# Kernel optimization log

Hardware: AMD Instinct MI355X
Metric: run time of the kernel (lower is better)

## Reference

```python
import jax, jax.numpy as jnp
import numpy as np

N, E = 50000, 640000          # nodes, edges
F_IN, HID, CLS = 128, 128, 64  # feature dims


def setup_inputs() -> dict:
    key = jax.random.key(0)
    ks = jax.random.split(key, 12)
    x = jax.random.normal(ks[0], (N, F_IN), dtype=jnp.float32)
    edge_index = jax.random.randint(ks[1], (2, E), 0, N, dtype=jnp.int32)
    s_in = 1.0 / np.sqrt(F_IN)
    s_h = 1.0 / np.sqrt(HID)
    return {
        "x": x,
        "edge_index": edge_index,
        "W0": jax.random.normal(ks[2], (F_IN, HID), jnp.float32) * s_in,
        "b0": jnp.zeros((HID,), jnp.float32),
        "W1": jax.random.normal(ks[3], (HID, HID), jnp.float32) * s_h,
        "b1": jnp.zeros((HID,), jnp.float32),
        "W2": jax.random.normal(ks[4], (HID, HID), jnp.float32) * s_h,
        "b2": jnp.zeros((HID,), jnp.float32),
        "W_lin": jax.random.normal(ks[5], (HID, CLS), jnp.float32) * s_h,
        "b_lin": jnp.zeros((CLS,), jnp.float32),
    }


def reference(x, edge_index, W0, b0, W1, b1, W2, b2, W_lin, b_lin):
    # GCNConv (PyG defaults): out = D^-1/2 (A + I) D^-1/2 (x @ W) + b
    row, col = edge_index[0], edge_index[1]  # source -> target
    # degree with self-loop (graph is fixed across layers, compute norms once)
    deg = jnp.zeros((N,), x.dtype).at[col].add(1.0) + 1.0
    dinv = jax.lax.rsqrt(deg)                 # deg >= 1, safe
    enorm = (dinv[row] * dinv[col])[:, None]  # [E,1] edge norm
    snorm = (dinv * dinv)[:, None]            # [N,1] self-loop norm

    def conv(h, W, b):
        h = h @ W                                             # [N,HID]
        agg = jnp.zeros_like(h).at[col].add(h[row] * enorm)   # neighbor agg
        return agg + h * snorm + b                            # + self loop + bias

    h = jax.nn.relu(conv(x, W0, b0))
    h = jax.nn.relu(conv(h, W1, b1))
    h = jax.nn.relu(conv(h, W2, b2))
    return h @ W_lin + b_lin
```

## Files before the change

kernel.cpp:

```cpp
#include <hip/hip_runtime.h>
#include <hip/hip_fp16.h>

#define N_NODES 50000
#define HID 128
#define CLS 64

#define NBINS 196
#define NBLK 256
#define LBUF_CAP 4096
#define WTOT 57344
#define GEMM0_BLOCKS 782
#define AROW 136

typedef __attribute__((ext_vector_type(8))) _Float16 f16x8;
typedef __attribute__((ext_vector_type(4))) float f32x4;

__global__ __launch_bounds__(256) void hist_wsplit_kernel(
    const int* __restrict__ col, int* __restrict__ hist,
    const float* __restrict__ W0, const float* __restrict__ W1,
    const float* __restrict__ W2, const float* __restrict__ Wl,
    __half* __restrict__ o0h, __half* __restrict__ o0l,
    __half* __restrict__ o1h, __half* __restrict__ o1l,
    __half* __restrict__ o2h, __half* __restrict__ o2l,
    __half* __restrict__ o3h, __half* __restrict__ o3l,
    int E, int chunk) {
    int widx = blockIdx.x * 256 + threadIdx.x;
    if (widx < WTOT) {
        const float* W;
        __half *oh, *ol;
        int NCdim, local;
        if (widx < 16384)      { W = W0; oh = o0h; ol = o0l; NCdim = 128; local = widx; }
        else if (widx < 32768) { W = W1; oh = o1h; ol = o1l; NCdim = 128; local = widx - 16384; }
        else if (widx < 49152) { W = W2; oh = o2h; ol = o2l; NCdim = 128; local = widx - 32768; }
        else                   { W = Wl; oh = o3h; ol = o3l; NCdim = 64;  local = widx - 49152; }
        int nn = local >> 7;
        int k = local & 127;
        float v = W[(size_t)k * NCdim + nn];
        __half h = __float2half_rn(v);
        oh[local] = h;
        ol[local] = __float2half_rn(v - __half2float(h));
    }
    __shared__ int h[NBINS];
    for (int i = threadIdx.x; i < NBINS; i += 256) h[i] = 0;
    __syncthreads();
    int b = blockIdx.x;
    int beg = b * chunk;
    int end = min(E, beg + chunk);
    if (beg < end) {
        int vend = beg + ((end - beg) & ~3);
        for (int i = beg + threadIdx.x * 4; i < vend; i += 1024) {
            int4 c4 = *(const int4*)(col + i);
            atomicAdd(&h[c4.x >> 8], 1);
            atomicAdd(&h[c4.y >> 8], 1);
            atomicAdd(&h[c4.z >> 8], 1);
            atomicAdd(&h[c4.w >> 8], 1);
        }
        int i = vend + threadIdx.x;
        if (i < end) atomicAdd(&h[col[i] >> 8], 1);
    }
    __syncthreads();
    for (int i = threadIdx.x; i < NBINS; i += 256)
        hist[i * NBLK + b] = h[i];
}

__global__ __launch_bounds__(256) void scatter_kernel(
    const int* __restrict__ row, const int* __restrict__ col,
    const int* __restrict__ hist, int* __restrict__ binBase_g,
    int* __restrict__ sbuf_src, unsigned char* __restrict__ sbuf_c,
    int E, int chunk) {
    __shared__ int sTot[256];
    __shared__ int cur[NBINS];
    int b = blockIdx.x, t = threadIdx.x;
    int partial = 0, total = 0;
    if (t < NBINS) {
        const int4* r4 = (const int4*)(hist + t * NBLK);
        int nb4 = b >> 2, rem = b & 3;
        for (int j = 0; j < NBLK / 4; ++j) {
            int4 v = r4[j];
            int s = v.x + v.y + v.z + v.w;
            total += s;
            if (j < nb4) partial += s;
            else if (j == nb4) {
                if (rem > 0) partial += v.x;
                if (rem > 1) partial += v.y;
                if (rem > 2) partial += v.z;
            }
        }
    }
    sTot[t] = (t < NBINS) ? total : 0;
    __syncthreads();
#pragma unroll
    for (int off = 1; off < 256; off <<= 1) {
        int u = (t >= off) ? sTot[t - off] : 0;
        __syncthreads();
        sTot[t] += u;
        __syncthreads();
    }
    int myBase = sTot[t] - total;
    if (t < NBINS) cur[t] = myBase + partial;
    if (b == 0) {
        if (t < NBINS) binBase_g[t] = myBase;
        if (t == 0) binBase_g[NBINS] = E;
    }
    __syncthreads();
    int beg = b * chunk;
    int end = min(E, beg + chunk);
    if (beg >= end) return;
    int vend = beg + ((end - beg) & ~3);
    for (int i = beg + t * 4; i < vend; i += 1024) {
        int4 c4 = *(const int4*)(col + i);
        int4 r4 = *(const int4*)(row + i);
        int p;
        p = atomicAdd(&cur[c4.x >> 8], 1); sbuf_src[p] = r4.x; sbuf_c[p] = (unsigned char)(c4.x & 255);
        p = atomicAdd(&cur[c4.y >> 8], 1); sbuf_src[p] = r4.y; sbuf_c[p] = (unsigned char)(c4.y & 255);
        p = atomicAdd(&cur[c4.z >> 8], 1); sbuf_src[p] = r4.z; sbuf_c[p] = (unsigned char)(c4.z & 255);
        p = atomicAdd(&cur[c4.w >> 8], 1); sbuf_src[p] = r4.w; sbuf_c[p] = (unsigned char)(c4.w & 255);
    }
    int i = vend + t;
    if (i < end) {
        int c = col[i];
        int p = atomicAdd(&cur[c >> 8], 1);
        sbuf_src[p] = row[i];
        sbuf_c[p] = (unsigned char)(c & 255);
    }
}

__device__ __forceinline__ void gemm0_body(
    const float* __restrict__ x, const __half* __restrict__ Bh,
    const __half* __restrict__ Bl, __half* __restrict__ C, int M, int rowTile) {
    constexpr int NT = 8;
    int lane = threadIdx.x & 63;
    int m0 = rowTile << 4;
    if (m0 >= M) return;
    int mr = lane & 15;
    int kq = (lane >> 4) << 3;

    const float*  af = x + (size_t)(m0 + mr) * 128 + kq;
    const __half* bh = Bh + (size_t)mr * 128 + kq;
    const __half* bl = Bl + (size_t)mr * 128 + kq;

    f32x4 acc[NT];
#pragma unroll
    for (int t = 0; t < NT; ++t) acc[t] = (f32x4){0.f, 0.f, 0.f, 0.f};
#pragma unroll
    for (int kc = 0; kc < 128; kc += 32) {
        float4 lo = *(const float4*)(af + kc);
        float4 hi = *(const float4*)(af + kc + 4);
        f16x8 a;
        a[0] = (_Float16)lo.x; a[1] = (_Float16)lo.y;
        a[2] = (_Float16)lo.z; a[3] = (_Float16)lo.w;
        a[4] = (_Float16)hi.x; a[5] = (_Float16)hi.y;
        a[6] = (_Float16)hi.z; a[7] = (_Float16)hi.w;
#pragma unroll
        for (int t = 0; t < NT; ++t) {
            f16x8 wh = *(const f16x8*)(bh + (size_t)t * 16 * 128 + kc);
            f16x8 wl = *(const f16x8*)(bl + (size_t)t * 16 * 128 + kc);
            acc[t] = __builtin_amdgcn_mfma_f32_16x16x32_f16(a, wh, acc[t], 0, 0, 0);
            acc[t] = __builtin_amdgcn_mfma_f32_16x16x32_f16(a, wl, acc[t], 0, 0, 0);
        }
    }
    int r0 = m0 + ((lane >> 4) << 2);
    int cc = lane & 15;
#pragma unroll
    for (int t = 0; t < NT; ++t)
#pragma unroll
        for (int r = 0; r < 4; ++r)
            C[(size_t)(r0 + r) * 128 + t * 16 + cc] =
                __float2half_rn(acc[t][r]);
}

__global__ __launch_bounds__(256) void csrplace_gemm0_kernel(
    const int* __restrict__ binBase,
    const int* __restrict__ sbuf_src, const unsigned char* __restrict__ sbuf_c,
    float* __restrict__ dinv, int* __restrict__ row_ptr, int* __restrict__ csr_src,
    const float* __restrict__ x, const __half* __restrict__ W0h,
    const __half* __restrict__ W0l, __half* __restrict__ h2, int n, int E) {
    __shared__ int lcnt[256];
    __shared__ int lcur[256];
    __shared__ int ss[256];
    __shared__ int lbuf[LBUF_CAP];
    int b = blockIdx.x;
    if (b >= NBINS) {
        gemm0_body(x, W0h, W0l, h2, n, (b - NBINS) * 4 + (threadIdx.x >> 6));
        return;
    }
    int t = threadIdx.x;
    lcnt[t] = 0;
    __syncthreads();
    int beg = binBase[b], end = binBase[b + 1];
    for (int j = beg + t; j < end; j += 256)
        atomicAdd(&lcnt[sbuf_c[j]], 1);
    __syncthreads();
    int deg = lcnt[t];
    int node = b * 256 + t;
    if (node < n) dinv[node] = rsqrtf((float)deg + 1.0f);
    ss[t] = deg;
    __syncthreads();
#pragma unroll
    for (int off = 1; off < 256; off <<= 1) {
        int u = (t >= off) ? ss[t - off] : 0;
        __syncthreads();
        ss[t] += u;
        __syncthreads();
    }
    int excl = ss[t] - deg;
    lcur[t] = excl;
    int total = ss[255];
    if (node < n) row_ptr[node] = beg + excl;
    if (b == 0 && t == 0) row_ptr[n] = E;
    __syncthreads();
    for (int j = beg + t; j < end; j += 256) {
        int c = sbuf_c[j];
        int pos = atomicAdd(&lcur[c], 1);
        lbuf[pos] = sbuf_src[j];
    }
    __syncthreads();
    for (int j = t; j < total; j += 256) csr_src[beg + j] = lbuf[j];
}

template<int NC, bool HEAD>
__global__ __launch_bounds__(256) void agg_gemm_kernel(
    const __half* __restrict__ h2, const int* __restrict__ row_ptr,
    const int* __restrict__ csr_src, const float* __restrict__ dinv,
    const float* __restrict__ bias,
    const __half* __restrict__ Bh, const __half* __restrict__ Bl,
    const float* __restrict__ gbias, void* __restrict__ Cv, int n) {
    __shared__ __half Als[16][AROW];
    int wave = threadIdx.x >> 6;
    int lane = threadIdx.x & 63;
    int loff = lane << 1;
    int m0 = blockIdx.x << 4;

#pragma unroll
    for (int k = 0; k < 4; ++k) {
        int lr = wave * 4 + k;
        int wid = m0 + lr;
        if (wid >= n) break;
        int beg = row_ptr[wid];
        int end = row_ptr[wid + 1];
        float dv = dinv[wid];
        float ax = 0.f, ay = 0.f;
        for (int base = beg; base < end; base += 64) {
            int cnt = end - base;
            if (cnt > 64) cnt = 64;
            int msrc = 0;
            float mw = 0.f;
            if (lane < cnt) {
                msrc = csr_src[base + lane];
                mw = dinv[msrc] * dv;
            }
            int j = 0;
            for (; j + 8 <= cnt; j += 8) {
                int s0 = __shfl(msrc, j),     s1 = __shfl(msrc, j + 1);
                int s2 = __shfl(msrc, j + 2), s3 = __shfl(msrc, j + 3);
                int s4 = __shfl(msrc, j + 4), s5 = __shfl(msrc, j + 5);
                int s6 = __shfl(msrc, j + 6), s7 = __shfl(msrc, j + 7);
                float w0 = __shfl(mw, j),     w1 = __shfl(mw, j + 1);
                float w2 = __shfl(mw, j + 2), w3 = __shfl(mw, j + 3);
                float w4 = __shfl(mw, j + 4), w5 = __shfl(mw, j + 5);
                float w6 = __shfl(mw, j + 6), w7 = __shfl(mw, j + 7);
                float2 v0 = __half22float2(*(const __half2*)(h2 + ((size_t)s0 << 7) + loff));
                float2 v1 = __half22float2(*(const __half2*)(h2 + ((size_t)s1 << 7) + loff));
                float2 v2 = __half22float2(*(const __half2*)(h2 + ((size_t)s2 << 7) + loff));
                float2 v3 = __half22float2(*(const __half2*)(h2 + ((size_t)s3 << 7) + loff));
                float2 v4 = __half22float2(*(const __half2*)(h2 + ((size_t)s4 << 7) + loff));
                float2 v5 = __half22float2(*(const __half2*)(h2 + ((size_t)s5 << 7) + loff));
                float2 v6 = __half22float2(*(const __half2*)(h2 + ((size_t)s6 << 7) + loff));
                float2 v7 = __half22float2(*(const __half2*)(h2 + ((size_t)s7 << 7) + loff));
                ax = fmaf(v0.x, w0, ax); ay = fmaf(v0.y, w0, ay);
                ax = fmaf(v1.x, w1, ax); ay = fmaf(v1.y, w1, ay);
                ax = fmaf(v2.x, w2, ax); ay = fmaf(v2.y, w2, ay);
                ax = fmaf(v3.x, w3, ax); ay = fmaf(v3.y, w3, ay);
                ax = fmaf(v4.x, w4, ax); ay = fmaf(v4.y, w4, ay);
                ax = fmaf(v5.x, w5, ax); ay = fmaf(v5.y, w5, ay);
                ax = fmaf(v6.x, w6, ax); ay = fmaf(v6.y, w6, ay);
                ax = fmaf(v7.x, w7, ax); ay = fmaf(v7.y, w7, ay);
            }
            for (; j + 4 <= cnt; j += 4) {
                int s0 = __shfl(msrc, j),     s1 = __shfl(msrc, j + 1);
                int s2 = __shfl(msrc, j + 2), s3 = __shfl(msrc, j + 3);
                float w0 = __shfl(mw, j),     w1 = __shfl(mw, j + 1);
                float w2 = __shfl(mw, j + 2), w3 = __shfl(mw, j + 3);
                float2 v0 = __half22float2(*(const __half2*)(h2 + ((size_t)s0 << 7) + loff));
                float2 v1 = __half22float2(*(const __half2*)(h2 + ((size_t)s1 << 7) + loff));
                float2 v2 = __half22float2(*(const __half2*)(h2 + ((size_t)s2 << 7) + loff));
                float2 v3 = __half22float2(*(const __half2*)(h2 + ((size_t)s3 << 7) + loff));
                ax = fmaf(v0.x, w0, ax); ay = fmaf(v0.y, w0, ay);
                ax = fmaf(v1.x, w1, ax); ay = fmaf(v1.y, w1, ay);
                ax = fmaf(v2.x, w2, ax); ay = fmaf(v2.y, w2, ay);
                ax = fmaf(v3.x, w3, ax); ay = fmaf(v3.y, w3, ay);
            }
            for (; j < cnt; ++j) {
                int s = __shfl(msrc, j);
                float w = __shfl(mw, j);
                float2 v = __half22float2(*(const __half2*)(h2 + ((size_t)s << 7) + loff));
                ax = fmaf(v.x, w, ax); ay = fmaf(v.y, w, ay);
            }
        }
        float sn = dv * dv;
        float2 self = __half22float2(*(const __half2*)(h2 + ((size_t)wid << 7) + loff));
        float2 b = *(const float2*)(bias + loff);
        float ox = fmaxf(fmaf(self.x, sn, ax) + b.x, 0.f);
        float oy = fmaxf(fmaf(self.y, sn, ay) + b.y, 0.f);
        *(__half2*)&Als[lr][loff] = __float22half2_rn(make_float2(ox, oy));
    }
    __syncthreads();

    constexpr int NT = NC / 16;
    constexpr int TPW = NT / 4;
    int mr = lane & 15;
    int kq = (lane >> 4) << 3;
    const __half* bh = Bh + (size_t)mr * 128 + kq;
    const __half* bl = Bl + (size_t)mr * 128 + kq;

    f32x4 acc[TPW];
#pragma unroll
    for (int t = 0; t < TPW; ++t) acc[t] = (f32x4){0.f, 0.f, 0.f, 0.f};
#pragma unroll
    for (int kc = 0; kc < 128; kc += 32) {
        f16x8 a = *(const f16x8*)&Als[mr][kq + kc];
#pragma unroll
        for (int t = 0; t < TPW; ++t) {
            int tile = wave * TPW + t;
            f16x8 wh = *(const f16x8*)(bh + (size_t)tile * 16 * 128 + kc);
            f16x8 wl = *(const f16x8*)(bl + (size_t)tile * 16 * 128 + kc);
            acc[t] = __builtin_amdgcn_mfma_f32_16x16x32_f16(a, wh, acc[t], 0, 0, 0);
            acc[t] = __builtin_amdgcn_mfma_f32_16x16x32_f16(a, wl, acc[t], 0, 0, 0);
        }
    }
    int r0 = m0 + ((lane >> 4) << 2);
    int cc = lane & 15;
#pragma unroll
    for (int t = 0; t < TPW; ++t) {
        int tile = wave * TPW + t;
        float bsv = HEAD ? gbias[tile * 16 + cc] : 0.f;
#pragma unroll
        for (int r = 0; r < 4; ++r) {
            if (r0 + r >= n) break;
            size_t idx = (size_t)(r0 + r) * NC + tile * 16 + cc;
            float val = acc[t][r] + bsv;
            if (HEAD)
                ((float*)Cv)[idx] = val;
            else
                ((__half*)Cv)[idx] = __float2half_rn(val);
        }
    }
}

extern "C" void kernel_launch(void* const* d_in, const int* in_sizes, int n_in,
                              void* d_out, int out_size, void* d_ws, size_t ws_size,
                              hipStream_t stream) {
    const float* x  = (const float*)d_in[0];
    const int* ei   = (const int*)d_in[1];
    const float* W0 = (const float*)d_in[2];
    const float* b0 = (const float*)d_in[3];
    const float* W1 = (const float*)d_in[4];
    const float* b1 = (const float*)d_in[5];
    const float* W2 = (const float*)d_in[6];
    const float* b2 = (const float*)d_in[7];
    const float* Wl = (const float*)d_in[8];
    const float* bl = (const float*)d_in[9];
    float* out = (float*)d_out;

    const int N = N_NODES;
    const int E = in_sizes[1] / 2;
    const int* row = ei;
    const int* col = ei + E;
    const int chunk = (((E + NBLK - 1) / NBLK) + 3) & ~3;

    char* ws = (char*)d_ws;
    auto alloc = [&](size_t bytes) {
        char* p = ws;
        ws += (bytes + 255) & ~(size_t)255;
        return p;
    };
    int*   hist    = (int*)alloc((size_t)NBINS * NBLK * 4);
    int*   binBase = (int*)alloc((size_t)(NBINS + 1) * 4);
    int*   sbuf_src= (int*)alloc((size_t)E * 4);
    unsigned char* sbuf_c = (unsigned char*)alloc((size_t)E);
    int*   row_ptr = (int*)alloc((size_t)(N + 1) * 4);
    float* dinv    = (float*)alloc((size_t)N * 4);
    int*   csr_src = (int*)alloc((size_t)E * 4);
    __half* h2a    = (__half*)alloc((size_t)N * HID * 2);
    __half* h2b    = (__half*)alloc((size_t)N * HID * 2);
    __half* Wt_h[4];
    __half* Wt_l[4];
    for (int i = 0; i < 3; ++i) {
        Wt_h[i] = (__half*)alloc((size_t)HID * HID * 2);
        Wt_l[i] = (__half*)alloc((size_t)HID * HID * 2);
    }
    Wt_h[3] = (__half*)alloc((size_t)CLS * HID * 2);
    Wt_l[3] = (__half*)alloc((size_t)CLS * HID * 2);

    hist_wsplit_kernel<<<NBLK, 256, 0, stream>>>(col, hist, W0, W1, W2, Wl,
        Wt_h[0], Wt_l[0], Wt_h[1], Wt_l[1], Wt_h[2], Wt_l[2], Wt_h[3], Wt_l[3], E, chunk);
    scatter_kernel<<<NBLK, 256, 0, stream>>>(row, col, hist, binBase, sbuf_src, sbuf_c, E, chunk);
    csrplace_gemm0_kernel<<<NBINS + GEMM0_BLOCKS, 256, 0, stream>>>(
        binBase, sbuf_src, sbuf_c, dinv, row_ptr, csr_src,
        x, Wt_h[0], Wt_l[0], h2a, N, E);

    const int fusedBlocks = (N + 15) / 16;

    agg_gemm_kernel<128, false><<<fusedBlocks, 256, 0, stream>>>(
        h2a, row_ptr, csr_src, dinv, b0, Wt_h[1], Wt_l[1], nullptr, h2b, N);
    agg_gemm_kernel<128, false><<<fusedBlocks, 256, 0, stream>>>(
        h2b, row_ptr, csr_src, dinv, b1, Wt_h[2], Wt_l[2], nullptr, h2a, N);
    agg_gemm_kernel<64, true><<<fusedBlocks, 256, 0, stream>>>(
        h2a, row_ptr, csr_src, dinv, b2, Wt_h[3], Wt_l[3], bl, out, N);
}
```

Before: 282.2 us.

## Aggregate four nodes per wave with 16-lane groups and 16-byte gathers

The neighbor aggregation previously processed one node per wave, looping serially over four nodes, with each lane loading one half2 (4 bytes) per neighbor. Now each wave splits into four 16-lane groups that handle four nodes concurrently, and each lane gathers 8 halves (16 bytes) per neighbor row into 8 accumulators. This aims to cut the serial per-node latency chain and raise the memory-level parallelism of the gathers. In exchange each lane holds more registers, and groups in the same wave diverge when their nodes have different degrees.

```diff
diff --git a/kernel.cpp b/kernel.cpp
--- a/kernel.cpp
+++ b/kernel.cpp
@@ -228,81 +228,89 @@
     __shared__ __half Als[16][AROW];
     int wave = threadIdx.x >> 6;
     int lane = threadIdx.x & 63;
-    int loff = lane << 1;
     int m0 = blockIdx.x << 4;
 
-#pragma unroll
-    for (int k = 0; k < 4; ++k) {
-        int lr = wave * 4 + k;
-        int wid = m0 + lr;
-        if (wid >= n) break;
+    int g = lane >> 4;
+    int l16 = lane & 15;
+    int baseLane = lane & 48;
+    int lr = (wave << 2) + g;
+    int wid = m0 + lr;
+    const __half* hrow = h2 + (l16 << 3);
+
+    if (wid < n) {
         int beg = row_ptr[wid];
         int end = row_ptr[wid + 1];
         float dv = dinv[wid];
-        float ax = 0.f, ay = 0.f;
-        for (int base = beg; base < end; base += 64) {
+        float acc[8];
+#pragma unroll
+        for (int i = 0; i < 8; ++i) acc[i] = 0.f;
+
+        for (int base = beg; base < end; base += 16) {
             int cnt = end - base;
-            if (cnt > 64) cnt = 64;
+            if (cnt > 16) cnt = 16;
             int msrc = 0;
             float mw = 0.f;
-            if (lane < cnt) {
-                msrc = csr_src[base + lane];
+            if (l16 < cnt) {
+                msrc = csr_src[base + l16];
                 mw = dinv[msrc] * dv;
             }
             int j = 0;
-            for (; j + 8 <= cnt; j += 8) {
-                int s0 = __shfl(msrc, j),     s1 = __shfl(msrc, j + 1);
-                int s2 = __shfl(msrc, j + 2), s3 = __shfl(msrc, j + 3);
-                int s4 = __shfl(msrc, j + 4), s5 = __shfl(msrc, j + 5);
-                int s6 = __shfl(msrc, j + 6), s7 = __shfl(msrc, j + 7);
-                float w0 = __shfl(mw, j),     w1 = __shfl(mw, j + 1);
-                float w2 = __shfl(mw, j + 2), w3 = __shfl(mw, j + 3);
-                float w4 = __shfl(mw, j + 4), w5 = __shfl(mw, j + 5);
-                float w6 = __shfl(mw, j + 6), w7 = __shfl(mw, j + 7);
-                float2 v0 = __half22float2(*(const __half2*)(h2 + ((size_t)s0 << 7) + loff));
-                float2 v1 = __half22float2(*(const __half2*)(h2 + ((size_t)s1 << 7) + loff));
-                float2 v2 = __half22float2(*(const __half2*)(h2 + ((size_t)s2 << 7) + loff));
-                float2 v3 = __half22float2(*(const __half2*)(h2 + ((size_t)s3 << 7) + loff));
-                float2 v4 = __half22float2(*(const __half2*)(h2 + ((size_t)s4 << 7) + loff));
-                float2 v5 = __half22float2(*(const __half2*)(h2 + ((size_t)s5 << 7) + loff));
-                float2 v6 = __half22float2(*(const __half2*)(h2 + ((size_t)s6 << 7) + loff));
-                float2 v7 = __half22float2(*(const __half2*)(h2 + ((size_t)s7 << 7) + loff));
-                ax = fmaf(v0.x, w0, ax); ay = fmaf(v0.y, w0, ay);
-                ax = fmaf(v1.x, w1, ax); ay = fmaf(v1.y, w1, ay);
-                ax = fmaf(v2.x, w2, ax); ay = fmaf(v2.y, w2, ay);
-                ax = fmaf(v3.x, w3, ax); ay = fmaf(v3.y, w3, ay);
-                ax = fmaf(v4.x, w4, ax); ay = fmaf(v4.y, w4, ay);
-                ax = fmaf(v5.x, w5, ax); ay = fmaf(v5.y, w5, ay);
-                ax = fmaf(v6.x, w6, ax); ay = fmaf(v6.y, w6, ay);
-                ax = fmaf(v7.x, w7, ax); ay = fmaf(v7.y, w7, ay);
+            for (; j + 4 <= cnt; j += 4) {
+                int s0 = __shfl(msrc, baseLane + j);
+                int s1 = __shfl(msrc, baseLane + j + 1);
+                int s2 = __shfl(msrc, baseLane + j + 2);
+                int s3 = __shfl(msrc, baseLane + j + 3);
+                float w0 = __shfl(mw, baseLane + j);
+                float w1 = __shfl(mw, baseLane + j + 1);
+                float w2 = __shfl(mw, baseLane + j + 2);
+                float w3 = __shfl(mw, baseLane + j + 3);
+                f16x8 v0 = *(const f16x8*)(hrow + ((size_t)s0 << 7));
+                f16x8 v1 = *(const f16x8*)(hrow + ((size_t)s1 << 7));
+                f16x8 v2 = *(const f16x8*)(hrow + ((size_t)s2 << 7));
+                f16x8 v3 = *(const f16x8*)(hrow + ((size_t)s3 << 7));
+#pragma unroll
+                for (int i = 0; i < 8; ++i) {
+                    acc[i] = fmaf((float)v0[i], w0, acc[i]);
+                    acc[i] = fmaf((float)v1[i], w1, acc[i]);
+                    acc[i] = fmaf((float)v2[i], w2, acc[i]);
+                    acc[i] = fmaf((float)v3[i], w3, acc[i]);
+                }
             }
-            for (; j + 4 <= cnt; j += 4) {
-                int s0 = __shfl(msrc, j),     s1 = __shfl(msrc, j + 1);
-                int s2 = __shfl(msrc, j + 2), s3 = __shfl(msrc, j + 3);
-                float w0 = __shfl(mw, j),     w1 = __shfl(mw, j + 1);
-                float w2 = __shfl(mw, j + 2), w3 = __shfl(mw, j + 3);
-                float2 v0 = __half22float2(*(const __half2*)(h2 + ((size_t)s0 << 7) + loff));
-                float2 v1 = __half22float2(*(const __half2*)(h2 + ((size_t)s1 << 7) + loff));
-                float2 v2 = __half22float2(*(const __half2*)(h2 + ((size_t)s2 << 7) + loff));
-                float2 v3 = __half22float2(*(const __half2*)(h2 + ((size_t)s3 << 7) + loff));
-                ax = fmaf(v0.x, w0, ax); ay = fmaf(v0.y, w0, ay);
-                ax = fmaf(v1.x, w1, ax); ay = fmaf(v1.y, w1, ay);
-                ax = fmaf(v2.x, w2, ax); ay = fmaf(v2.y, w2, ay);
-                ax = fmaf(v3.x, w3, ax); ay = fmaf(v3.y, w3, ay);
+            for (; j + 2 <= cnt; j += 2) {
+                int s0 = __shfl(msrc, baseLane + j);
+                int s1 = __shfl(msrc, baseLane + j + 1);
+                float w0 = __shfl(mw, baseLane + j);
+                float w1 = __shfl(mw, baseLane + j + 1);
+                f16x8 v0 = *(const f16x8*)(hrow + ((size_t)s0 << 7));
+                f16x8 v1 = *(const f16x8*)(hrow + ((size_t)s1 << 7));
+#pragma unroll
+                for (int i = 0; i < 8; ++i) {
+                    acc[i] = fmaf((float)v0[i], w0, acc[i]);
+                    acc[i] = fmaf((float)v1[i], w1, acc[i]);
+                }
             }
-            for (; j < cnt; ++j) {
-                int s = __shfl(msrc, j);
-                float w = __shfl(mw, j);
-                float2 v = __half22float2(*(const __half2*)(h2 + ((size_t)s << 7) + loff));
-                ax = fmaf(v.x, w, ax); ay = fmaf(v.y, w, ay);
+            if (j < cnt) {
+                int s0 = __shfl(msrc, baseLane + j);
+                float w0 = __shfl(mw, baseLane + j);
+                f16x8 v0 = *(const f16x8*)(hrow + ((size_t)s0 << 7));
+#pragma unroll
+                for (int i = 0; i < 8; ++i)
+                    acc[i] = fmaf((float)v0[i], w0, acc[i]);
             }
         }
         float sn = dv * dv;
-        float2 self = __half22float2(*(const __half2*)(h2 + ((size_t)wid << 7) + loff));
-        float2 b = *(const float2*)(bias + loff);
-        float ox = fmaxf(fmaf(self.x, sn, ax) + b.x, 0.f);
-        float oy = fmaxf(fmaf(self.y, sn, ay) + b.y, 0.f);
-        *(__half2*)&Als[lr][loff] = __float22half2_rn(make_float2(ox, oy));
+        f16x8 sv = *(const f16x8*)(hrow + ((size_t)wid << 7));
+        float4 ba = *(const float4*)(bias + (l16 << 3));
+        float4 bb = *(const float4*)(bias + (l16 << 3) + 4);
+        float o[8];
+#pragma unroll
+        for (int i = 0; i < 8; ++i) o[i] = fmaf((float)sv[i], sn, acc[i]);
+        o[0] += ba.x; o[1] += ba.y; o[2] += ba.z; o[3] += ba.w;
+        o[4] += bb.x; o[5] += bb.y; o[6] += bb.z; o[7] += bb.w;
+        f16x8 pk;
+#pragma unroll
+        for (int i = 0; i < 8; ++i) pk[i] = (_Float16)fmaxf(o[i], 0.f);
+        *(f16x8*)&Als[lr][l16 << 3] = pk;
     }
     __syncthreads();
 
```

Measured after the change: 268.9 us. 1.05x faster.
